# Kernel tuning notes

Measured on AMD Instinct MI355X. Metric: run time of the kernel, lower is better.

The kernel has to match this reference:

```python
import jax, jax.numpy as jnp
import numpy as np

B, S, D, H, HD, FF, L = 16384, 5, 6, 2, 3, 2048, 4
EPS = 1e-5


def setup_inputs() -> dict:
    key = jax.random.key(0)
    ks = jax.random.split(key, 20)
    s = lambda fan: 1.0 / np.sqrt(fan)
    inp = {
        'x': jax.random.normal(ks[0], (B, S, D), dtype=jnp.float32),
        # per-layer stacked MHA params (in_proj split into q/k/v) and out_proj
        'Wq': jax.random.uniform(ks[1], (L, D, D), jnp.float32, -s(D), s(D)),
        'bq': jax.random.uniform(ks[2], (L, D), jnp.float32, -s(D), s(D)),
        'Wk': jax.random.uniform(ks[3], (L, D, D), jnp.float32, -s(D), s(D)),
        'bk': jax.random.uniform(ks[4], (L, D), jnp.float32, -s(D), s(D)),
        'Wv': jax.random.uniform(ks[5], (L, D, D), jnp.float32, -s(D), s(D)),
        'bv': jax.random.uniform(ks[6], (L, D), jnp.float32, -s(D), s(D)),
        'Wo': jax.random.uniform(ks[7], (L, D, D), jnp.float32, -s(D), s(D)),
        'bo': jax.random.uniform(ks[8], (L, D), jnp.float32, -s(D), s(D)),
        # FFN: linear1 D->FF, linear2 FF->D (torch Linear stores [out,in])
        'W1': jax.random.uniform(ks[9], (L, FF, D), jnp.float32, -s(D), s(D)),
        'b1': jax.random.uniform(ks[10], (L, FF), jnp.float32, -s(D), s(D)),
        'W2': jax.random.uniform(ks[11], (L, D, FF), jnp.float32, -s(FF), s(FF)),
        'b2': jax.random.uniform(ks[12], (L, D), jnp.float32, -s(FF), s(FF)),
        # layernorms
        'g1': jnp.ones((L, D), jnp.float32),
        'be1': jnp.zeros((L, D), jnp.float32),
        'g2': jnp.ones((L, D), jnp.float32),
        'be2': jnp.zeros((L, D), jnp.float32),
        # classification head Linear(30, 2)
        'Wfc': jax.random.uniform(ks[13], (2, S * D), jnp.float32, -s(S * D), s(S * D)),
        'bfc': jax.random.uniform(ks[14], (2,), jnp.float32, -s(S * D), s(S * D)),
    }
    return inp


def _layernorm(x, g, b):
    m = jnp.mean(x, axis=-1, keepdims=True)
    v = jnp.mean(jnp.square(x - m), axis=-1, keepdims=True)
    return (x - m) * jax.lax.rsqrt(v + EPS) * g + b


def _encoder_stack(x, Wq, bq, Wk, bk, Wv, bv, Wo, bo, W1, b1, W2, b2, g1, be1, g2, be2):
    scale = 1.0 / np.sqrt(HD)
    for i in range(L):  # small fixed loop over layers
        # multi-head self-attention (post-norm, eval mode: dropout = identity)
        q = (x @ Wq[i].T + bq[i]).reshape(B, S, H, HD)
        k = (x @ Wk[i].T + bk[i]).reshape(B, S, H, HD)
        v = (x @ Wv[i].T + bv[i]).reshape(B, S, H, HD)
        scores = jnp.einsum('bqhd,bkhd->bhqk', q, k) * scale
        attn = jax.nn.softmax(scores, axis=-1)
        ctx = jnp.einsum('bhqk,bkhd->bqhd', attn, v).reshape(B, S, D)
        x = _layernorm(x + ctx @ Wo[i].T + bo[i], g1[i], be1[i])
        # FFN: relu(x W1^T + b1) W2^T + b2
        h = jax.nn.relu(x @ W1[i].T + b1[i])  # [B,S,FF]
        x = _layernorm(x + h @ W2[i].T + b2[i], g2[i], be2[i])
    return x


def reference(x, Wq, bq, Wk, bk, Wv, bv, Wo, bo, W1, b1, W2, b2, g1, be1, g2, be2, Wfc, bfc):
    t = _encoder_stack(x, Wq, bq, Wk, bk, Wv, bv, Wo, bo, W1, b1, W2, b2, g1, be1, g2, be2)
    flat = t.reshape(-1, S * D)
    logits = flat @ Wfc.T + bfc
    return jax.nn.softmax(logits, axis=1)
```

## Files before the change

kernel.cpp:

```cpp
#include <hip/hip_runtime.h>
#include <math.h>

#define NL 4
#define NBATCH 16384
#define NS 5
#define ND 6
#define NH 2
#define NHD 3
#define NFF 2048
#define EPSV 1e-5f

#define ITEMS 16
#define TPB 256
#define NPAIR 64
#define ROW (NS * ND)
#define NVAL (ITEMS * ROW)

#define W1K_N (NL * NPAIR * 2 * 16)
#define W2K_N (NL * NPAIR * 4 * 6)

typedef __fp16 v8h __attribute__((ext_vector_type(8)));
typedef __fp16 v2h __attribute__((ext_vector_type(2)));
typedef float f32x4 __attribute__((ext_vector_type(4)));

union HU8 { uint4 u; v8h h; __fp16 f[8]; };

__device__ inline unsigned pk_u32(float a, float b) {
    union { v2h h; unsigned u; } x;
    x.h = __builtin_amdgcn_cvt_pkrtz(a, b);
    return x.u;
}
__device__ inline unsigned packh(float a, float b) {
    union { __fp16 h[2]; unsigned u; } x;
    x.h[0] = (__fp16)a; x.h[1] = (__fp16)b; return x.u;
}

__device__ __align__(16) uint4 W1K[W1K_N];
__device__ __align__(16) uint4 W2K[W2K_N + 64];

__global__ void pack_kernel(const float* __restrict__ W1,
                            const float* __restrict__ b1,
                            const float* __restrict__ W2) {
    int idx = blockIdx.x * 256 + threadIdx.x;
    if (idx < W1K_N) {
        int r = idx & 15, t = (idx >> 4) & 1, p = (idx >> 5) & 63, l = idx >> 11;
        int j = (2 * p + t) * 16 + r;
        uint4 o;
        o.x = packh(W1[(size_t)(l * NFF + j) * ND + 0], W1[(size_t)(l * NFF + j) * ND + 1]);
        o.y = packh(W1[(size_t)(l * NFF + j) * ND + 2], W1[(size_t)(l * NFF + j) * ND + 3]);
        o.z = packh(W1[(size_t)(l * NFF + j) * ND + 4], W1[(size_t)(l * NFF + j) * ND + 5]);
        o.w = packh(b1[l * NFF + j], 0.f);
        W1K[idx] = o;
    } else if (idx < W1K_N + W2K_N) {
        int t = idx - W1K_N;
        int r = t % 6; int t6 = t / 6;
        int g = t6 & 3, p = (t6 >> 2) & 63, l = t6 >> 8;
        HU8 o;
#pragma unroll
        for (int e = 0; e < 8; ++e) {
            int j = p * 32 + ((e < 4) ? (4 * g + e) : (16 + 4 * g + e - 4));
            o.f[e] = (__fp16)W2[(size_t)(l * ND + r) * NFF + j];
        }
        W2K[t] = o.u;
    }
}

__global__ __launch_bounds__(TPB)
__attribute__((amdgpu_waves_per_eu(4, 4)))
void encoder_kernel(
    const float* __restrict__ xin,
    const float* __restrict__ Wq, const float* __restrict__ bq,
    const float* __restrict__ Wk, const float* __restrict__ bk,
    const float* __restrict__ Wv, const float* __restrict__ bv,
    const float* __restrict__ Wo, const float* __restrict__ bo,
    const float* __restrict__ b2,
    const float* __restrict__ g1, const float* __restrict__ be1,
    const float* __restrict__ g2, const float* __restrict__ be2,
    const float* __restrict__ Wfc, const float* __restrict__ bfc,
    float* __restrict__ out) {
    __shared__ float xs[NVAL];
    __shared__ float ybuf[4 * 5 * 32 * 4];
    __shared__ float kvs[ITEMS * NS * 2 * ND];

    const int tid = threadIdx.x;
    const int base = blockIdx.x * ITEMS;

    if (tid < NVAL / 4)
        ((float4*)xs)[tid] = ((const float4*)(xin + (size_t)base * ROW))[tid];
    __syncthreads();

    const bool act = tid < ITEMS * NS;
    const int ai = tid / NS;
    const int at = tid - ai * NS;

    const int lane = tid & 63;
    const int jq = tid >> 6;
    const int c16 = lane & 15, g = lane >> 4;

    v8h z8; z8 = (v8h)(__fp16)0.f;
    const f32x4 cz = {0.f, 0.f, 0.f, 0.f};
    const uint4 u4z = make_uint4(0u, 0u, 0u, 0u);

    for (int l = 0; l < NL; ++l) {
        const uint4* p1 = W1K + (size_t)(l * NPAIR + jq * 16) * 32 + c16;
        const uint4* p2 = W2K + ((size_t)(l * NPAIR + jq * 16) * 4 + g) * 6 + c16;
        uint4 wa[2][2], wb[2][2], ww[2][2];
#pragma unroll
        for (int bb = 0; bb < 2; ++bb)
#pragma unroll
            for (int pp = 0; pp < 2; ++pp) {
                const int pr = bb * 2 + pp;
                wa[bb][pp] = u4z; wb[bb][pp] = u4z; ww[bb][pp] = u4z;
                if (g == 0) {
                    wa[bb][pp] = p1[pr * 32];
                    wb[bb][pp] = p1[pr * 32 + 16];
                }
                if (c16 < 6) ww[bb][pp] = p2[pr * 24];
            }

        float xr[ND], qv[ND];
        if (act) {
#pragma unroll
            for (int d = 0; d < ND; ++d) xr[d] = xs[(ai * NS + at) * ND + d];
#pragma unroll
            for (int d = 0; d < ND; ++d) {
                float aq = bq[l * ND + d], ak = bk[l * ND + d], av = bv[l * ND + d];
#pragma unroll
                for (int e = 0; e < ND; ++e) {
                    aq += Wq[(l * ND + d) * ND + e] * xr[e];
                    ak += Wk[(l * ND + d) * ND + e] * xr[e];
                    av += Wv[(l * ND + d) * ND + e] * xr[e];
                }
                qv[d] = aq;
                kvs[(ai * NS + at) * 2 * ND + d] = ak;
                kvs[(ai * NS + at) * 2 * ND + ND + d] = av;
            }
        }
        __syncthreads();
        if (act) {
            const float scale = 0.57735026919f;
            float ctx[ND];
#pragma unroll
            for (int h = 0; h < NH; ++h) {
                float sc[NS];
                float mx = -1e30f;
#pragma unroll
                for (int u = 0; u < NS; ++u) {
                    float s = 0.f;
#pragma unroll
                    for (int d = 0; d < NHD; ++d)
                        s += qv[h * NHD + d] * kvs[(ai * NS + u) * 2 * ND + h * NHD + d];
                    s *= scale;
                    sc[u] = s;
                    mx = fmaxf(mx, s);
                }
                float sum = 0.f;
#pragma unroll
                for (int u = 0; u < NS; ++u) {
                    sc[u] = __expf(sc[u] - mx);
                    sum += sc[u];
                }
                float inv = 1.f / sum;
#pragma unroll
                for (int d = 0; d < NHD; ++d) {
                    float cx = 0.f;
#pragma unroll
                    for (int u = 0; u < NS; ++u)
                        cx += sc[u] * kvs[(ai * NS + u) * 2 * ND + ND + h * NHD + d];
                    ctx[h * NHD + d] = cx * inv;
                }
            }
            float yr[ND];
#pragma unroll
            for (int d = 0; d < ND; ++d) {
                float a = bo[l * ND + d];
#pragma unroll
                for (int e = 0; e < ND; ++e) a += Wo[(l * ND + d) * ND + e] * ctx[e];
                yr[d] = a + xr[d];
            }
            float m = 0.f;
#pragma unroll
            for (int d = 0; d < ND; ++d) m += yr[d];
            m *= (1.f / ND);
            float va = 0.f;
#pragma unroll
            for (int d = 0; d < ND; ++d) { float dv = yr[d] - m; va += dv * dv; }
            va *= (1.f / ND);
            float r = rsqrtf(va + EPSV);
#pragma unroll
            for (int d = 0; d < ND; ++d)
                xs[(ai * NS + at) * ND + d] =
                    (yr[d] - m) * r * g1[l * ND + d] + be1[l * ND + d];
        }
        __syncthreads();
        v8h xb[5];
#pragma unroll
        for (int mt = 0; mt < 5; ++mt) {
            HU8 ux; ux.u = u4z;
            if (g == 0) {
                int row = mt * 16 + c16;
                const float* xp = &xs[row * ND];
                ux.u.x = pk_u32(xp[0], xp[1]);
                ux.u.y = pk_u32(xp[2], xp[3]);
                ux.u.z = pk_u32(xp[4], xp[5]);
                ux.u.w = 0x00003c00u;
            }
            xb[mt] = ux.h;
        }
        f32x4 y0 = cz, y1 = cz, y2 = cz, y3 = cz, y4 = cz;
        __builtin_amdgcn_s_setprio(1);
#pragma unroll
        for (int gq = 0; gq < 8; ++gq) {
            const int cur = gq & 1;
#pragma unroll
            for (int pp = 0; pp < 2; ++pp) {
                HU8 a1; a1.u = wa[cur][pp];
                HU8 b1f; b1f.u = wb[cur][pp];
                HU8 w2f; w2f.u = ww[cur][pp];
#define FFN_STEP(YREG, XB)                                                      \
                {                                                               \
                    f32x4 h0 = __builtin_amdgcn_mfma_f32_16x16x32_f16(          \
                        a1.h, (XB), cz, 0, 0, 0);                               \
                    f32x4 h1 = __builtin_amdgcn_mfma_f32_16x16x32_f16(          \
                        b1f.h, (XB), cz, 0, 0, 0);                              \
                    HU8 hb;                                                     \
                    hb.u.x = pk_u32(h0.x, h0.y);                                \
                    hb.u.y = pk_u32(h0.z, h0.w);                                \
                    hb.u.z = pk_u32(h1.x, h1.y);                                \
                    hb.u.w = pk_u32(h1.z, h1.w);                                \
                    hb.h = __builtin_elementwise_max(hb.h, z8);                 \
                    YREG = __builtin_amdgcn_mfma_f32_16x16x32_f16(              \
                        w2f.h, hb.h, YREG, 0, 0, 0);                            \
                }
                FFN_STEP(y0, xb[0])
                FFN_STEP(y1, xb[1])
                FFN_STEP(y2, xb[2])
                FFN_STEP(y3, xb[3])
                FFN_STEP(y4, xb[4])
#undef FFN_STEP
            }
            if (gq < 6) {
#pragma unroll
                for (int pp = 0; pp < 2; ++pp) {
                    const int pr = (gq + 2) * 2 + pp;
                    uint4 na = u4z, nb = u4z, nw = u4z;
                    if (g == 0) {
                        na = p1[pr * 32];
                        nb = p1[pr * 32 + 16];
                    }
                    if (c16 < 6) nw = p2[pr * 24];
                    wa[cur][pp] = na; wb[cur][pp] = nb; ww[cur][pp] = nw;
                }
            }
        }
        __builtin_amdgcn_s_setprio(0);
        if (lane < 32) {
            f32x4* yb4 = (f32x4*)ybuf;
            int sb = (jq * 5) * 32 + lane;
            yb4[sb + 0 * 32] = y0;
            yb4[sb + 1 * 32] = y1;
            yb4[sb + 2 * 32] = y2;
            yb4[sb + 3 * 32] = y3;
            yb4[sb + 4 * 32] = y4;
        }
        __syncthreads();
        if (act) {
            int R = ai * NS + at;
            int mtR = R >> 4, cR = R & 15;
            float yr[ND];
#pragma unroll
            for (int d = 0; d < ND; ++d) {
                int gR = d >> 2, iR = d & 3;
                float s = 0.f;
#pragma unroll
                for (int q = 0; q < 4; ++q)
                    s += ybuf[((q * 5 + mtR) * 32 + gR * 16 + cR) * 4 + iR];
                yr[d] = xs[R * ND + d] + s + b2[l * ND + d];
            }
            float m = 0.f;
#pragma unroll
            for (int d = 0; d < ND; ++d) m += yr[d];
            m *= (1.f / ND);
            float va = 0.f;
#pragma unroll
            for (int d = 0; d < ND; ++d) { float dv = yr[d] - m; va += dv * dv; }
            va *= (1.f / ND);
            float r = rsqrtf(va + EPSV);
#pragma unroll
            for (int d = 0; d < ND; ++d)
                xs[R * ND + d] = (yr[d] - m) * r * g2[l * ND + d] + be2[l * ND + d];
        }
        __syncthreads();
    }
    if (tid < ITEMS) {
        float l0 = bfc[0], l1 = bfc[1];
#pragma unroll
        for (int v = 0; v < ROW; ++v) {
            float xv = xs[tid * ROW + v];
            l0 += Wfc[v] * xv;
            l1 += Wfc[ROW + v] * xv;
        }
        float mx = fmaxf(l0, l1);
        float e0 = __expf(l0 - mx), e1 = __expf(l1 - mx);
        float inv = 1.f / (e0 + e1);
        out[(size_t)(base + tid) * 2 + 0] = e0 * inv;
        out[(size_t)(base + tid) * 2 + 1] = e1 * inv;
    }
}

extern "C" void kernel_launch(void* const* d_in, const int* in_sizes, int n_in,
                              void* d_out, int out_size, void* d_ws, size_t ws_size,
                              hipStream_t stream) {
    (void)in_sizes; (void)n_in; (void)d_ws; (void)ws_size; (void)out_size;
    const float* x = (const float*)d_in[0];
    const float* Wq = (const float*)d_in[1];
    const float* bq = (const float*)d_in[2];
    const float* Wk = (const float*)d_in[3];
    const float* bk = (const float*)d_in[4];
    const float* Wv = (const float*)d_in[5];
    const float* bv = (const float*)d_in[6];
    const float* Wo = (const float*)d_in[7];
    const float* bo = (const float*)d_in[8];
    const float* W1 = (const float*)d_in[9];
    const float* b1 = (const float*)d_in[10];
    const float* W2 = (const float*)d_in[11];
    const float* b2 = (const float*)d_in[12];
    const float* g1 = (const float*)d_in[13];
    const float* be1 = (const float*)d_in[14];
    const float* g2 = (const float*)d_in[15];
    const float* be2 = (const float*)d_in[16];
    const float* Wfc = (const float*)d_in[17];
    const float* bfc = (const float*)d_in[18];
    float* out = (float*)d_out;

    const int npack = W1K_N + W2K_N;
    hipLaunchKernelGGL(pack_kernel, dim3((npack + 255) / 256), dim3(256), 0, stream,
                       W1, b1, W2);
    hipLaunchKernelGGL(encoder_kernel, dim3(NBATCH / ITEMS), dim3(TPB), 0, stream,
                       x, Wq, bq, Wk, bk, Wv, bv, Wo, bo, b2, g1, be1, g2, be2,
                       Wfc, bfc, out);
}
```

Baseline: 71.27 us.

## Stream packed FFN weights into LDS via async global_load_lds double buffering

Repacks W1/W2 FFN weights into contiguous 4KB chunks per layer, wave and chunk, then streams them into a per-wave double-buffered LDS region using global_load_lds. Each wave waits on vmcnt before reading fragments from LDS, replacing the earlier register-held global prefetch. The aim is fewer vector registers and wider, coalesced weight fetches. The cost is LDS traffic, extra LDS capacity (32KB per block) and manual waitcnt handling, which may reduce occupancy or add stalls.

```diff
diff --git a/kernel.cpp b/kernel.cpp
--- a/kernel.cpp
+++ b/kernel.cpp
@@ -16,8 +16,7 @@
 #define ROW (NS * ND)
 #define NVAL (ITEMS * ROW)
 
-#define W1K_N (NL * NPAIR * 2 * 16)
-#define W2K_N (NL * NPAIR * 4 * 6)
+#define NCHUNK (NL * 4 * 4)
 
 typedef __fp16 v8h __attribute__((ext_vector_type(8)));
 typedef __fp16 v2h __attribute__((ext_vector_type(2)));
@@ -34,40 +33,46 @@
     union { __fp16 h[2]; unsigned u; } x;
     x.h[0] = (__fp16)a; x.h[1] = (__fp16)b; return x.u;
 }
-
-__device__ __align__(16) uint4 W1K[W1K_N];
-__device__ __align__(16) uint4 W2K[W2K_N + 64];
+__device__ inline void gload16(const void* g, void* l) {
+    __builtin_amdgcn_global_load_lds(
+        (const __attribute__((address_space(1))) unsigned int*)g,
+        (__attribute__((address_space(3))) unsigned int*)l, 16, 0, 0);
+}
+
+__device__ __align__(16) uint4 BLOB[NCHUNK * 256];
 
 __global__ void pack_kernel(const float* __restrict__ W1,
                             const float* __restrict__ b1,
                             const float* __restrict__ W2) {
     int idx = blockIdx.x * 256 + threadIdx.x;
-    if (idx < W1K_N) {
-        int r = idx & 15, t = (idx >> 4) & 1, p = (idx >> 5) & 63, l = idx >> 11;
-        int j = (2 * p + t) * 16 + r;
-        uint4 o;
+    if (idx >= NCHUNK * 256) return;
+    int rec = idx & 255, c = idx >> 8;
+    int ch = c & 3, jq = (c >> 2) & 3, l = c >> 4;
+    uint4 o = make_uint4(0u, 0u, 0u, 0u);
+    if (rec < 128) {
+        int i = rec >> 5, t = (rec >> 4) & 1, r = rec & 15;
+        int p = jq * 16 + ch * 4 + i;
+        int j = p * 32 + t * 16 + r;
         o.x = packh(W1[(size_t)(l * NFF + j) * ND + 0], W1[(size_t)(l * NFF + j) * ND + 1]);
         o.y = packh(W1[(size_t)(l * NFF + j) * ND + 2], W1[(size_t)(l * NFF + j) * ND + 3]);
         o.z = packh(W1[(size_t)(l * NFF + j) * ND + 4], W1[(size_t)(l * NFF + j) * ND + 5]);
         o.w = packh(b1[l * NFF + j], 0.f);
-        W1K[idx] = o;
-    } else if (idx < W1K_N + W2K_N) {
-        int t = idx - W1K_N;
-        int r = t % 6; int t6 = t / 6;
-        int g = t6 & 3, p = (t6 >> 2) & 63, l = t6 >> 8;
-        HU8 o;
+    } else if (rec < 224) {
+        int q = rec - 128;
+        int i = q / 24, g = (q % 24) / 6, r = q % 6;
+        int p = jq * 16 + ch * 4 + i;
+        HU8 t8; t8.u = o;
 #pragma unroll
         for (int e = 0; e < 8; ++e) {
             int j = p * 32 + ((e < 4) ? (4 * g + e) : (16 + 4 * g + e - 4));
-            o.f[e] = (__fp16)W2[(size_t)(l * ND + r) * NFF + j];
-        }
-        W2K[t] = o.u;
+            t8.f[e] = (__fp16)W2[(size_t)(l * ND + r) * NFF + j];
+        }
+        o = t8.u;
     }
-}
-
-__global__ __launch_bounds__(TPB)
-__attribute__((amdgpu_waves_per_eu(4, 4)))
-void encoder_kernel(
+    BLOB[idx] = o;
+}
+
+__global__ __launch_bounds__(TPB, 4) void encoder_kernel(
     const float* __restrict__ xin,
     const float* __restrict__ Wq, const float* __restrict__ bq,
     const float* __restrict__ Wk, const float* __restrict__ bk,
@@ -81,6 +86,7 @@
     __shared__ float xs[NVAL];
     __shared__ float ybuf[4 * 5 * 32 * 4];
     __shared__ float kvs[ITEMS * NS * 2 * ND];
+    __shared__ uint4 wlds[4][2][256];
 
     const int tid = threadIdx.x;
     const int base = blockIdx.x * ITEMS;
@@ -102,21 +108,10 @@
     const uint4 u4z = make_uint4(0u, 0u, 0u, 0u);
 
     for (int l = 0; l < NL; ++l) {
-        const uint4* p1 = W1K + (size_t)(l * NPAIR + jq * 16) * 32 + c16;
-        const uint4* p2 = W2K + ((size_t)(l * NPAIR + jq * 16) * 4 + g) * 6 + c16;
-        uint4 wa[2][2], wb[2][2], ww[2][2];
-#pragma unroll
-        for (int bb = 0; bb < 2; ++bb)
-#pragma unroll
-            for (int pp = 0; pp < 2; ++pp) {
-                const int pr = bb * 2 + pp;
-                wa[bb][pp] = u4z; wb[bb][pp] = u4z; ww[bb][pp] = u4z;
-                if (g == 0) {
-                    wa[bb][pp] = p1[pr * 32];
-                    wb[bb][pp] = p1[pr * 32 + 16];
-                }
-                if (c16 < 6) ww[bb][pp] = p2[pr * 24];
-            }
+        const char* gsl = (const char*)BLOB + (size_t)((l * 4 + jq) * 4) * 4096;
+#pragma unroll
+        for (int it = 0; it < 4; ++it)
+            gload16(gsl + it * 1024 + lane * 16, (char*)&wlds[jq][0][0] + it * 1024);
 
         float xr[ND], qv[ND];
         if (act) {
@@ -210,13 +205,29 @@
         f32x4 y0 = cz, y1 = cz, y2 = cz, y3 = cz, y4 = cz;
         __builtin_amdgcn_s_setprio(1);
 #pragma unroll
-        for (int gq = 0; gq < 8; ++gq) {
-            const int cur = gq & 1;
-#pragma unroll
-            for (int pp = 0; pp < 2; ++pp) {
-                HU8 a1; a1.u = wa[cur][pp];
-                HU8 b1f; b1f.u = wb[cur][pp];
-                HU8 w2f; w2f.u = ww[cur][pp];
+        for (int ch = 0; ch < 4; ++ch) {
+            const int cur = ch & 1;
+            if (ch < 3) {
+                const char* gn = gsl + (size_t)(ch + 1) * 4096;
+#pragma unroll
+                for (int it = 0; it < 4; ++it)
+                    gload16(gn + it * 1024 + lane * 16,
+                            (char*)&wlds[jq][cur ^ 1][0] + it * 1024);
+                asm volatile("s_waitcnt vmcnt(4)" ::: "memory");
+            } else {
+                asm volatile("s_waitcnt vmcnt(0)" ::: "memory");
+            }
+#pragma unroll
+            for (int i = 0; i < 4; ++i) {
+                HU8 a1; a1.u = u4z;
+                HU8 b1f; b1f.u = u4z;
+                HU8 w2f; w2f.u = u4z;
+                if (g == 0) {
+                    a1.u  = wlds[jq][cur][i * 32 + c16];
+                    b1f.u = wlds[jq][cur][i * 32 + 16 + c16];
+                }
+                if (c16 < 6)
+                    w2f.u = wlds[jq][cur][128 + i * 24 + g * 6 + c16];
 #define FFN_STEP(YREG, XB)                                                      \
                 {                                                               \
                     f32x4 h0 = __builtin_amdgcn_mfma_f32_16x16x32_f16(          \
@@ -238,19 +249,6 @@
                 FFN_STEP(y3, xb[3])
                 FFN_STEP(y4, xb[4])
 #undef FFN_STEP
-            }
-            if (gq < 6) {
-#pragma unroll
-                for (int pp = 0; pp < 2; ++pp) {
-                    const int pr = (gq + 2) * 2 + pp;
-                    uint4 na = u4z, nb = u4z, nw = u4z;
-                    if (g == 0) {
-                        na = p1[pr * 32];
-                        nb = p1[pr * 32 + 16];
-                    }
-                    if (c16 < 6) nw = p2[pr * 24];
-                    wa[cur][pp] = na; wb[cur][pp] = nb; ww[cur][pp] = nw;
-                }
             }
         }
         __builtin_amdgcn_s_setprio(0);
@@ -333,7 +331,7 @@
     const float* bfc = (const float*)d_in[18];
     float* out = (float*)d_out;
 
-    const int npack = W1K_N + W2K_N;
+    const int npack = NCHUNK * 256;
     hipLaunchKernelGGL(pack_kernel, dim3((npack + 255) / 256), dim3(256), 0, stream,
                        W1, b1, W2);
     hipLaunchKernelGGL(encoder_kernel, dim3(NBATCH / ITEMS), dim3(TPB), 0, stream,
```

Measured after the change: 90.28 us. +26.7%, slower.
